# Kernel tuning notes

Hardware: AMD Instinct MI355X
Metric: run time of the kernel (lower is better)

Reference implementation:

```python
import jax, jax.numpy as jnp
import numpy as np


def _per_patch_bce(logits, labels):
    # numerically stable BCE-with-logits, mean over (C,H,W) -> per-patch loss
    bce = jnp.maximum(logits, 0.0) - logits * labels + jnp.log1p(jnp.exp(-jnp.abs(logits)))
    return bce.mean(axis=(-3, -2, -1))


def setup_inputs() -> dict:
    key = jax.random.key(0)
    k1, k2 = jax.random.split(key)
    B, C, N, M = 64, 1, 128, 136
    inputs = jax.random.normal(k1, (B, C, N, N), dtype=jnp.float32)   # logits
    targets = jax.random.uniform(k2, (B, C, M, M), dtype=jnp.float32)  # soft labels in [0,1]
    return {"inputs": inputs, "targets": targets}


def reference(inputs, targets):
    B, C, N1, N2 = inputs.shape
    M1, M2 = targets.shape[-2], targets.shape[-1]
    s1 = M1 - N1 + 1
    s2 = M2 - N2 + 1
    S = s1 * s2
    center_flat = (s1 // 2) * s2 + (s2 // 2)

    # all (i,j) shift offsets, row-major to match i*shift2+j flattening
    ii, jj = jnp.meshgrid(jnp.arange(s1), jnp.arange(s2), indexing="ij")
    shifts = jnp.stack([ii.ravel(), jj.ravel()], axis=-1)  # (S, 2)

    def extract(ij):
        return jax.lax.dynamic_slice(targets, (0, 0, ij[0], ij[1]), (B, C, N1, N2))

    windows = jax.vmap(extract)(shifts)            # (S, B, C, N, N)
    err = _per_patch_bce(inputs[None], windows)    # (S, B)
    err = err.T                                    # (B, S)

    min_loss = err.min(axis=1)                     # (B,)
    min_ij = err.argmin(axis=1)                    # (B,) first-min tiebreak, as torch.min
    # prefer the center shift when it ties the minimum
    center_is_min = err[:, center_flat] == min_loss
    min_ij = jnp.where(center_is_min, center_flat, min_ij)

    total_loss = min_loss.sum()
    adjusted_labels = windows[min_ij, jnp.arange(B)]  # (B, C, N, N)
    row_shifts = min_ij // s2
    col_shifts = min_ij % s2
    return total_loss, adjusted_labels, (row_shifts, col_shifts)
```

## Files before the change

### kernel.cpp

```cpp
#include <hip/hip_runtime.h>
#include <math.h>

#define B 64
#define N 128
#define M 136
#define S2 9
#define S 81
#define NPIX (N*N)
#define MPIX (M*M)
#define CENTER 40
#define MF4 34
#define YF4 4624

__device__ __forceinline__ float softplus_f(float x) {
    float t = __expf(-fabsf(x));
    return fmaxf(x, 0.0f) + __logf(1.0f + t);
}

#define ROR_ADD(x, CTRL) ((x) + __int_as_float(__builtin_amdgcn_update_dpp( \
        0, __float_as_int(x), (CTRL), 0xf, 0xf, true)))

template <int O>
__device__ __forceinline__ void gather2(const float4* yl4, float* dstB,
                                        int q, int tid, int i2, int j2) {
    #pragma unroll
    for (int k2 = 0; k2 < 2; ++k2) {
        int Q = q * 1024 + tid + 512 * k2;
        int row = (Q >> 5) + i2;
        int i0 = (Q & 31) + (j2 >> 2);
        float4 A = yl4[row * MF4 + i0];
        float r0, r1, r2, r3;
        if (O == 0) { r0 = A.x; r1 = A.y; r2 = A.z; r3 = A.w; }
        else {
            float4 Bq = yl4[row * MF4 + i0 + 1];
            if (O == 1)      { r0 = A.y; r1 = A.z; r2 = A.w; r3 = Bq.x; }
            else if (O == 2) { r0 = A.z; r1 = A.w; r2 = Bq.x; r3 = Bq.y; }
            else             { r0 = A.w; r1 = Bq.x; r2 = Bq.y; r3 = Bq.z; }
        }
        float* d = dstB + 4 * Q;
        d[0] = r0; d[1] = r1; d[2] = r2; d[3] = r3;
    }
}

__global__ __launch_bounds__(512, 1) void k_all(const float* __restrict__ x,
                                                const float* __restrict__ y,
                                                float* __restrict__ out) {
    const int tid = threadIdx.x;
    const int b = blockIdx.x & 63;
    const int q = blockIdx.x >> 6;

    __shared__ float ylds[MPIX];
    __shared__ float part[32][84];
    __shared__ float dsum[S];
    __shared__ float spart[8];
    __shared__ int sij;

    const float4* yl4 = (const float4*)ylds;
    const float4* yg4 = (const float4*)(y + (size_t)b * MPIX);
    const float4* xg4 = (const float4*)(x + (size_t)b * NPIX);

    const int cq = tid & 31;
    const int rbt = (tid >> 5) * 8;

    float4 xp0 = xg4[(rbt + 0) * 32 + cq];
    float4 xp1 = xg4[(rbt + 1) * 32 + cq];
    float4 xp2 = xg4[(rbt + 2) * 32 + cq];
    float4 xp3 = xg4[(rbt + 3) * 32 + cq];

    {
        float4* yd = (float4*)ylds;
        #pragma unroll
        for (int t = 0; t < 10; ++t) {
            int idx = tid + 512 * t;
            if (idx < YF4) yd[idx] = yg4[idx];
        }
    }
    __syncthreads();

    float acc[S];
    #pragma unroll
    for (int s = 0; s < S; ++s) acc[s] = 0.0f;
    float sp = 0.0f;

    #pragma unroll 1
    for (int k = 0; k < 2; ++k) {
        const int xrb = rbt + k * 4;
        float4 xc0, xc1, xc2, xc3;
        if (k == 0) { xc0 = xp0; xc1 = xp1; xc2 = xp2; xc3 = xp3; }
        else {
            xc0 = xg4[(xrb + 0) * 32 + cq];
            xc1 = xg4[(xrb + 1) * 32 + cq];
            xc2 = xg4[(xrb + 2) * 32 + cq];
            xc3 = xg4[(xrb + 3) * 32 + cq];
        }

        if (q == 0) {
            sp += softplus_f(xc0.x) + softplus_f(xc0.y) + softplus_f(xc0.z) + softplus_f(xc0.w)
                + softplus_f(xc1.x) + softplus_f(xc1.y) + softplus_f(xc1.z) + softplus_f(xc1.w)
                + softplus_f(xc2.x) + softplus_f(xc2.y) + softplus_f(xc2.z) + softplus_f(xc2.w)
                + softplus_f(xc3.x) + softplus_f(xc3.y) + softplus_f(xc3.z) + softplus_f(xc3.w);
        }

        const int yrb = xrb;
        #pragma unroll
        for (int rr = 0; rr < 12; ++rr) {
            const float4* yrow = yl4 + (yrb + rr) * MF4 + cq;
            float4 A = yrow[0];
            float4 Bq = yrow[1];
            float4 Cq = yrow[2];
            float ya[12];
            ya[0] = A.x;  ya[1] = A.y;  ya[2] = A.z;  ya[3] = A.w;
            ya[4] = Bq.x; ya[5] = Bq.y; ya[6] = Bq.z; ya[7] = Bq.w;
            ya[8] = Cq.x; ya[9] = Cq.y; ya[10] = Cq.z; ya[11] = Cq.w;
            #pragma unroll
            for (int v = 0; v < 4; ++v) {
                const int ii = rr - v;
                if (ii >= 0 && ii <= 8) {
                    const float4 xv = (v == 0) ? xc0 : (v == 1) ? xc1
                                    : (v == 2) ? xc2 : xc3;
                    #pragma unroll
                    for (int j = 0; j < 9; ++j) {
                        acc[ii * 9 + j] += xv.x * ya[j]     + xv.y * ya[j + 1]
                                         + xv.z * ya[j + 2] + xv.w * ya[j + 3];
                    }
                }
            }
        }
    }

    #pragma unroll
    for (int s = 0; s < S; ++s) {
        float v = acc[s];
        v = ROR_ADD(v, 0x128);
        v = ROR_ADD(v, 0x124);
        v = ROR_ADD(v, 0x122);
        v = ROR_ADD(v, 0x121);
        acc[s] = v;
    }
    if ((tid & 15) == 0) {
        const int g = tid >> 4;
        #pragma unroll
        for (int s = 0; s < S; ++s) part[g][s] = acc[s];
    }
    if (q == 0) {
        #pragma unroll
        for (int m = 1; m < 64; m <<= 1) sp += __shfl_xor(sp, m, 64);
        if ((tid & 63) == 0) spart[tid >> 6] = sp;
    }
    __syncthreads();

    if (tid < S) {
        float s0 = 0.0f;
        #pragma unroll
        for (int g = 0; g < 32; ++g) s0 += part[g][tid];
        dsum[tid] = s0;
    }
    __syncthreads();

    if (tid == 0) {
        float best = -INFINITY; int bi = 0;
        for (int s = 0; s < S; ++s) {
            float d = dsum[s];
            if (d > best) { best = d; bi = s; }
        }
        if (dsum[CENTER] == best) bi = CENTER;
        sij = bi;
        if (q == 0) {
            out[1 + B * NPIX + b]     = (float)(bi / S2);
            out[1 + B * NPIX + B + b] = (float)(bi % S2);
            float P = 0.0f;
            #pragma unroll
            for (int w = 0; w < 8; ++w) P += spart[w];
            atomicAdd(out, (P - best) * (1.0f / (float)NPIX));
        }
    }
    __syncthreads();

    {
        const int ij = sij;
        const int i2 = ij / S2, j2 = ij - i2 * S2;
        float* dstB = out + 1 + (size_t)b * NPIX;
        const int o = j2 & 3;
        if (o == 0)      gather2<0>(yl4, dstB, q, tid, i2, j2);
        else if (o == 1) gather2<1>(yl4, dstB, q, tid, i2, j2);
        else if (o == 2) gather2<2>(yl4, dstB, q, tid, i2, j2);
        else             gather2<3>(yl4, dstB, q, tid, i2, j2);
    }
}

extern "C" void kernel_launch(void* const* d_in, const int* in_sizes, int n_in,
                              void* d_out, int out_size, void* d_ws, size_t ws_size,
                              hipStream_t stream) {
    const float* x = (const float*)d_in[0];
    const float* y = (const float*)d_in[1];
    float* out = (float*)d_out;

    k_all<<<dim3(B * 4), 512, 0, stream>>>(x, y, out);
}
```

Before: 80.07 us.

## Use async global-to-LDS loads, preload x, double-buffer LDS rows, parallel argmax

Copies the target tile into shared memory with direct global_load_lds instructions instead of register-staged loads. Preloads all eight x rows up front rather than loading the second half inside the loop. Software-pipelines the shared-memory row reads with a two-slot buffer, and replaces the single-thread argmax over 81 shifts with a wave-level shuffle reduction. The aim is to cut load latency and serial tail work, at the cost of higher register pressure from the extra buffers.

```diff
diff --git a/kernel.cpp b/kernel.cpp
--- a/kernel.cpp
+++ b/kernel.cpp
@@ -62,18 +62,21 @@
     const int cq = tid & 31;
     const int rbt = (tid >> 5) * 8;
 
-    float4 xp0 = xg4[(rbt + 0) * 32 + cq];
-    float4 xp1 = xg4[(rbt + 1) * 32 + cq];
-    float4 xp2 = xg4[(rbt + 2) * 32 + cq];
-    float4 xp3 = xg4[(rbt + 3) * 32 + cq];
+    float4 xq[8];
+    #pragma unroll
+    for (int r = 0; r < 8; ++r) xq[r] = xg4[(rbt + r) * 32 + cq];
 
     {
         float4* yd = (float4*)ylds;
         #pragma unroll
-        for (int t = 0; t < 10; ++t) {
+        for (int t = 0; t < 9; ++t) {
             int idx = tid + 512 * t;
-            if (idx < YF4) yd[idx] = yg4[idx];
-        }
+            __builtin_amdgcn_global_load_lds(
+                (const __attribute__((address_space(1))) void*)(yg4 + idx),
+                (__attribute__((address_space(3))) void*)(yd + idx),
+                16, 0, 0);
+        }
+        if (tid < 16) yd[4608 + tid] = yg4[4608 + tid];
     }
     __syncthreads();
 
@@ -84,15 +87,10 @@
 
     #pragma unroll 1
     for (int k = 0; k < 2; ++k) {
-        const int xrb = rbt + k * 4;
-        float4 xc0, xc1, xc2, xc3;
-        if (k == 0) { xc0 = xp0; xc1 = xp1; xc2 = xp2; xc3 = xp3; }
-        else {
-            xc0 = xg4[(xrb + 0) * 32 + cq];
-            xc1 = xg4[(xrb + 1) * 32 + cq];
-            xc2 = xg4[(xrb + 2) * 32 + cq];
-            xc3 = xg4[(xrb + 3) * 32 + cq];
-        }
+        float4 xc0 = xq[k * 4 + 0];
+        float4 xc1 = xq[k * 4 + 1];
+        float4 xc2 = xq[k * 4 + 2];
+        float4 xc3 = xq[k * 4 + 3];
 
         if (q == 0) {
             sp += softplus_f(xc0.x) + softplus_f(xc0.y) + softplus_f(xc0.z) + softplus_f(xc0.w)
@@ -101,17 +99,23 @@
                 + softplus_f(xc3.x) + softplus_f(xc3.y) + softplus_f(xc3.z) + softplus_f(xc3.w);
         }
 
-        const int yrb = xrb;
+        const int yrb = rbt + k * 4;
+        float4 Ab[2], Bb[2], Cb[2];
+        {
+            const float4* y0 = yl4 + yrb * MF4 + cq;
+            Ab[0] = y0[0]; Bb[0] = y0[1]; Cb[0] = y0[2];
+        }
         #pragma unroll
         for (int rr = 0; rr < 12; ++rr) {
-            const float4* yrow = yl4 + (yrb + rr) * MF4 + cq;
-            float4 A = yrow[0];
-            float4 Bq = yrow[1];
-            float4 Cq = yrow[2];
+            const int cur = rr & 1, nxt = cur ^ 1;
+            if (rr < 11) {
+                const float4* yn = yl4 + (yrb + rr + 1) * MF4 + cq;
+                Ab[nxt] = yn[0]; Bb[nxt] = yn[1]; Cb[nxt] = yn[2];
+            }
             float ya[12];
-            ya[0] = A.x;  ya[1] = A.y;  ya[2] = A.z;  ya[3] = A.w;
-            ya[4] = Bq.x; ya[5] = Bq.y; ya[6] = Bq.z; ya[7] = Bq.w;
-            ya[8] = Cq.x; ya[9] = Cq.y; ya[10] = Cq.z; ya[11] = Cq.w;
+            ya[0] = Ab[cur].x;  ya[1] = Ab[cur].y;  ya[2] = Ab[cur].z;  ya[3] = Ab[cur].w;
+            ya[4] = Bb[cur].x;  ya[5] = Bb[cur].y;  ya[6] = Bb[cur].z;  ya[7] = Bb[cur].w;
+            ya[8] = Cb[cur].x;  ya[9] = Cb[cur].y;  ya[10] = Cb[cur].z; ya[11] = Cb[cur].w;
             #pragma unroll
             for (int v = 0; v < 4; ++v) {
                 const int ii = rr - v;
@@ -157,21 +161,30 @@
     }
     __syncthreads();
 
-    if (tid == 0) {
-        float best = -INFINITY; int bi = 0;
-        for (int s = 0; s < S; ++s) {
-            float d = dsum[s];
-            if (d > best) { best = d; bi = s; }
-        }
-        if (dsum[CENTER] == best) bi = CENTER;
-        sij = bi;
-        if (q == 0) {
-            out[1 + B * NPIX + b]     = (float)(bi / S2);
-            out[1 + B * NPIX + B + b] = (float)(bi % S2);
-            float P = 0.0f;
-            #pragma unroll
-            for (int w = 0; w < 8; ++w) P += spart[w];
-            atomicAdd(out, (P - best) * (1.0f / (float)NPIX));
+    if (tid < 64) {
+        float bv = dsum[tid];
+        int   bi = tid;
+        if (tid < S - 64) {
+            float v2 = dsum[64 + tid];
+            if (v2 > bv) { bv = v2; bi = 64 + tid; }
+        }
+        #pragma unroll
+        for (int m = 1; m < 64; m <<= 1) {
+            float ov = __shfl_xor(bv, m, 64);
+            int   oi = __shfl_xor(bi, m, 64);
+            if (ov > bv || (ov == bv && oi < bi)) { bv = ov; bi = oi; }
+        }
+        if (tid == 0) {
+            if (dsum[CENTER] == bv) bi = CENTER;
+            sij = bi;
+            if (q == 0) {
+                out[1 + B * NPIX + b]     = (float)(bi / S2);
+                out[1 + B * NPIX + B + b] = (float)(bi % S2);
+                float P = 0.0f;
+                #pragma unroll
+                for (int w = 0; w < 8; ++w) P += spart[w];
+                atomicAdd(out, (P - bv) * (1.0f / (float)NPIX));
+            }
         }
     }
     __syncthreads();
```

Measured after the change: 90.98 us. +13.6%, slower.
